# Kernel tuning notes

Measured on AMD Instinct MI355X. Metric: run time of the kernel, lower is better.

## Reference

```python
import jax, jax.numpy as jnp
import numpy as np

D_MODEL = 256
TOP_K = 32


def setup_inputs() -> dict:
    key = jax.random.key(0)
    k1, k2, k3 = jax.random.split(key, 3)
    query = jax.random.normal(k1, (4, 512, D_MODEL), dtype=jnp.float32)
    keys = jax.random.normal(k2, (65536, D_MODEL), dtype=jnp.float32)
    values = jax.random.normal(k3, (65536, D_MODEL), dtype=jnp.float32)
    return {"query": query, "keys": keys, "values": values}


def reference(query, keys, values):
    # query: [B, C, d], keys: [M, d], values: [M, d]
    reverse = False
    scale = D_MODEL ** (-0.5)
    scores = jnp.einsum("bcd,md->bcm", query, keys) * scale  # [B, C, M]
    if reverse:
        scores = -scores
    topk_scores, topk_indices = jax.lax.top_k(scores, TOP_K)  # [B, C, K]
    attn_weights = jax.nn.softmax(topk_scores, axis=-1)       # [B, C, K]
    retrieved = values[topk_indices]                           # [B, C, K, d]
    if reverse:
        retrieved = -retrieved
    aggregated = jnp.einsum("bckd,bck->bcd", retrieved, attn_weights)
    return aggregated
```

## Files before the change

### kernel.cpp

```cpp
#include <hip/hip_runtime.h>
#include <math.h>

#define D_MODEL 256
#define NQ 2048
#define M_KEYS 65536
#define CAP 512
#define RESCORE 64
#define TOPK 32
#define ZTHRESH 2.8f
#define QT 128
#define KPB 1024
#define KSTEP 32
#define NSTEP (KPB / KSTEP)
#define CAPQ 14

typedef _Float16 half8v __attribute__((ext_vector_type(8)));
typedef _Float16 half4v __attribute__((ext_vector_type(4)));
typedef float floatx4 __attribute__((ext_vector_type(4)));

__device__ __forceinline__ void async_load16(const _Float16* g, _Float16* l) {
  __builtin_amdgcn_global_load_lds(
      (const __attribute__((address_space(1))) void*)g,
      (__attribute__((address_space(3))) void*)l, 16, 0, 0);
}

__device__ __forceinline__ void issue_tile(const _Float16* __restrict__ kh, int row0,
                                           int sr0, int schunk, _Float16* dst, int tid) {
  const _Float16* src = kh + (size_t)(row0 + sr0) * D_MODEL + (schunk << 3);
  _Float16* d = dst + tid * 8;
#pragma unroll
  for (int jj = 0; jj < 4; ++jj)
    async_load16(src + (size_t)(jj * 8) * D_MODEL, d + jj * 2048);
}

__global__ __launch_bounds__(256) void cvt_f32_f16(const float* __restrict__ src,
                                                   _Float16* __restrict__ dst, int n4) {
  int i = blockIdx.x * 256 + threadIdx.x;
  if (i < n4) {
    const float4 v = ((const float4*)src)[i];
    half4v h = {(_Float16)v.x, (_Float16)v.y, (_Float16)v.z, (_Float16)v.w};
    ((half4v*)dst)[i] = h;
  }
}

__global__ __launch_bounds__(256) void qtau_kernel(const float* __restrict__ qf,
                                                   float* __restrict__ qtau) {
  const int lane = threadIdx.x & 63;
  const int q = blockIdx.x * 4 + (threadIdx.x >> 6);
  const float4 v = ((const float4*)(qf + (size_t)q * D_MODEL))[lane];
  float ss = v.x * v.x + v.y * v.y + v.z * v.z + v.w * v.w;
#pragma unroll
  for (int off = 32; off > 0; off >>= 1) ss += __shfl_down(ss, off);
  if (lane == 0) qtau[q] = ZTHRESH * sqrtf(ss);
}

__global__ __launch_bounds__(256, 2) void phase1_kernel(
    const _Float16* __restrict__ qh, const _Float16* __restrict__ kh,
    const float* __restrict__ qtau,
    float* __restrict__ cand_s, int* __restrict__ cand_i, int* __restrict__ cnt) {
  __shared__ __align__(16) char smem[65536];
  _Float16* qstage = (_Float16*)smem;
  _Float16* buf0 = (_Float16*)smem;
  _Float16* buf1 = (_Float16*)(smem + 16384);
  _Float16* buf2 = (_Float16*)(smem + 32768);
  float* qs = (float*)(smem + 49152);
  int* qi = (int*)(smem + 56320);
  int* qcnt = (int*)(smem + 63488);

  const int tid = threadIdx.x;
  const int lane = tid & 63;
  const int wave = tid >> 6;

  const int bid = blockIdx.x;
  const int xcd = bid & 7;
  const int j = bid >> 3;
  const int qbase = (j & 15) * QT;
  const int kstart0 = (xcd * 8 + (j >> 4)) * KPB;

  const int sr0 = tid >> 5;
  const int schunk = (tid & 31) ^ sr0;

  {
    const _Float16* src = qh + (size_t)(qbase + sr0) * D_MODEL + (schunk << 3);
    _Float16* d = qstage + tid * 8;
#pragma unroll
    for (int jj = 0; jj < 16; ++jj)
      async_load16(src + (size_t)(jj * 8) * D_MODEL, d + jj * 2048);
  }
  __syncthreads();

  const int lrow = lane & 15;
  const int g4 = lane >> 4;
  const int wr = wave << 5;
  const int lx = lrow & 7;

  half8v a[2][8];
#pragma unroll
  for (int mi = 0; mi < 2; ++mi) {
    const int row = wr + mi * 16 + lrow;
#pragma unroll
    for (int kk = 0; kk < 8; ++kk) {
      const int sw = ((kk << 2) + g4) ^ lx;
      a[mi][kk] = *(const half8v*)&qstage[row * D_MODEL + (sw << 3)];
    }
  }

  const int qrow0 = qbase + wr + (g4 << 2);
  float tq[8];
#pragma unroll
  for (int mi = 0; mi < 2; ++mi)
#pragma unroll
    for (int r = 0; r < 4; ++r)
      tq[mi * 4 + r] = qtau[qrow0 + mi * 16 + r];

  __syncthreads();

  if (tid < QT) qcnt[tid] = 0;

  issue_tile(kh, kstart0, sr0, schunk, buf0, tid);
  issue_tile(kh, kstart0 + KSTEP, sr0, schunk, buf1, tid);

  _Float16 *rdb = buf0, *nxb = buf1, *pfb = buf2;

#pragma unroll 1
  for (int s = 0; s < NSTEP; ++s) {
    if (s + 1 < NSTEP) {
      asm volatile("s_waitcnt vmcnt(4)" ::: "memory");
    } else {
      asm volatile("s_waitcnt vmcnt(0)" ::: "memory");
    }
    __builtin_amdgcn_s_barrier();
    __builtin_amdgcn_sched_barrier(0);

    if (s + 2 < NSTEP)
      issue_tile(kh, kstart0 + (s + 2) * KSTEP, sr0, schunk, pfb, tid);

    floatx4 acc[2][2] = {};
    __builtin_amdgcn_s_setprio(1);
#pragma unroll
    for (int kk = 0; kk < 8; ++kk) {
      const int sw = ((kk << 2) + g4) ^ lx;
      const half8v b0 = *(const half8v*)&rdb[lrow * D_MODEL + (sw << 3)];
      const half8v b1 = *(const half8v*)&rdb[(16 + lrow) * D_MODEL + (sw << 3)];
      acc[0][0] = __builtin_amdgcn_mfma_f32_16x16x32_f16(a[0][kk], b0, acc[0][0], 0, 0, 0);
      acc[0][1] = __builtin_amdgcn_mfma_f32_16x16x32_f16(a[0][kk], b1, acc[0][1], 0, 0, 0);
      acc[1][0] = __builtin_amdgcn_mfma_f32_16x16x32_f16(a[1][kk], b0, acc[1][0], 0, 0, 0);
      acc[1][1] = __builtin_amdgcn_mfma_f32_16x16x32_f16(a[1][kk], b1, acc[1][1], 0, 0, 0);
    }
    __builtin_amdgcn_s_setprio(0);

    const int kglob0 = kstart0 + s * KSTEP;
    const int qloc0 = wr + (g4 << 2);
#pragma unroll
    for (int mi = 0; mi < 2; ++mi) {
#pragma unroll
      for (int ni = 0; ni < 2; ++ni) {
#pragma unroll
        for (int r = 0; r < 4; ++r) {
          const float dot = acc[mi][ni][r];
          if (dot > tq[mi * 4 + r]) {
            const int ql = qloc0 + mi * 16 + r;
            const int kidx = kglob0 + ni * 16 + lrow;
            int p = atomicAdd(&qcnt[ql], 1);
            if (p < CAPQ) {
              qs[ql * CAPQ + p] = dot * 0.0625f;
              qi[ql * CAPQ + p] = kidx;
            } else {
              int pos = atomicAdd(&cnt[qbase + ql], 1);
              if (pos < CAP) {
                cand_s[(size_t)(qbase + ql) * CAP + pos] = dot * 0.0625f;
                cand_i[(size_t)(qbase + ql) * CAP + pos] = kidx;
              }
            }
          }
        }
      }
    }

    _Float16* t = rdb; rdb = nxb; nxb = pfb; pfb = t;
  }

  __syncthreads();
  if (tid < QT) {
    int n = qcnt[tid];
    if (n > CAPQ) n = CAPQ;
    if (n > 0) {
      const int q = qbase + tid;
      int base = atomicAdd(&cnt[q], n);
#pragma unroll 2
      for (int jj = 0; jj < n; ++jj) {
        int p = base + jj;
        if (p < CAP) {
          cand_s[(size_t)q * CAP + p] = qs[tid * CAPQ + jj];
          cand_i[(size_t)q * CAP + p] = qi[tid * CAPQ + jj];
        }
      }
    }
  }
}

__global__ __launch_bounds__(256) void phase2_kernel(
    const float* __restrict__ qf, const float* __restrict__ keys,
    const float* __restrict__ vals, const float* __restrict__ cand_s,
    const int* __restrict__ cand_i, const int* __restrict__ cnt,
    float* __restrict__ out) {
  __shared__ float sc[CAP];
  __shared__ int si[CAP];
  __shared__ float xs[RESCORE];
  __shared__ int xi[RESCORE];
  __shared__ float ew[TOPK];
  __shared__ float invsum;

  const int qid = blockIdx.x;
  const int tid = threadIdx.x;
  int c = cnt[qid];
  if (c > CAP) c = CAP;
  const int n = (c <= 256) ? 256 : CAP;

  for (int i = tid; i < n; i += 256) {
    bool valid = (i < c);
    sc[i] = valid ? cand_s[(size_t)qid * CAP + i] : -1e30f;
    si[i] = valid ? cand_i[(size_t)qid * CAP + i] : -1;
  }

  for (int k = 2; k <= n; k <<= 1) {
    for (int j = k >> 1; j > 0; j >>= 1) {
      __syncthreads();
      for (int t = tid; t < n; t += 256) {
        int p = t ^ j;
        if (p > t) {
          float a = sc[t], b = sc[p];
          bool desc = ((t & k) == 0);
          if (desc ? (a < b) : (a > b)) {
            sc[t] = b; sc[p] = a;
            int tmp = si[t]; si[t] = si[p]; si[p] = tmp;
          }
        }
      }
    }
  }
  __syncthreads();

  const int lane = tid & 63, wv = tid >> 6;
  const float4 qv = ((const float4*)(qf + (size_t)qid * D_MODEL))[lane];
#pragma unroll 4
  for (int cand = wv; cand < RESCORE; cand += 4) {
    int kidx = si[cand];
    float sres = -1e30f;
    if (kidx >= 0) {
      const float4 kv = ((const float4*)(keys + (size_t)kidx * D_MODEL))[lane];
      double p = (double)qv.x * kv.x + (double)qv.y * kv.y +
                 (double)qv.z * kv.z + (double)qv.w * kv.w;
#pragma unroll
      for (int off = 32; off > 0; off >>= 1) p += __shfl_down(p, off);
      sres = (float)(p * 0.0625);
    }
    if (lane == 0) { xs[cand] = sres; xi[cand] = kidx; }
  }
  __syncthreads();

  for (int k = 2; k <= RESCORE; k <<= 1) {
    for (int j = k >> 1; j > 0; j >>= 1) {
      __syncthreads();
      if (tid < RESCORE) {
        int t = tid, p = t ^ j;
        if (p > t) {
          float a = xs[t], b = xs[p];
          bool desc = ((t & k) == 0);
          if (desc ? (a < b) : (a > b)) {
            xs[t] = b; xs[p] = a;
            int tmp = xi[t]; xi[t] = xi[p]; xi[p] = tmp;
          }
        }
      }
    }
  }
  __syncthreads();

  if (tid < TOPK) ew[tid] = expf(xs[tid] - xs[0]);
  __syncthreads();
  if (tid == 0) {
    float s = 0.f;
    for (int i = 0; i < TOPK; ++i) s += ew[i];
    invsum = 1.0f / s;
  }
  __syncthreads();

  float acc = 0.f;
#pragma unroll
  for (int i = 0; i < TOPK; ++i)
    acc += (ew[i] * invsum) * vals[(size_t)xi[i] * D_MODEL + tid];
  out[(size_t)qid * D_MODEL + tid] = acc;
}

extern "C" void kernel_launch(void* const* d_in, const int* in_sizes, int n_in,
                              void* d_out, int out_size, void* d_ws, size_t ws_size,
                              hipStream_t stream) {
  const float* q = (const float*)d_in[0];
  const float* k = (const float*)d_in[1];
  const float* v = (const float*)d_in[2];
  float* out = (float*)d_out;

  char* ws = (char*)d_ws;
  _Float16* kh = (_Float16*)ws;
  _Float16* qh = (_Float16*)(ws + 33554432);
  float* cand_s = (float*)(ws + 34603008);
  int* cand_i = (int*)(ws + 38797312);
  int* cnt = (int*)(ws + 42991616);
  float* qtau = (float*)(ws + 42999808);

  hipMemsetAsync(cnt, 0, NQ * sizeof(int), stream);
  cvt_f32_f16<<<(M_KEYS * D_MODEL / 4 + 255) / 256, 256, 0, stream>>>(k, kh, M_KEYS * D_MODEL / 4);
  cvt_f32_f16<<<(NQ * D_MODEL / 4 + 255) / 256, 256, 0, stream>>>(q, qh, NQ * D_MODEL / 4);
  qtau_kernel<<<NQ / 4, 256, 0, stream>>>(q, qtau);

  phase1_kernel<<<(NQ / QT) * (M_KEYS / KPB), 256, 0, stream>>>(qh, kh, qtau, cand_s, cand_i, cnt);
  phase2_kernel<<<NQ, 256, 0, stream>>>(q, k, v, cand_s, cand_i, cnt, out);
}
```

Measured before the change: 285.6 us.

## Restructure phase1 into per-wave independent key streams with packed hit pool

Phase1 now has each wave stream its own 1024-key range through a private triple buffer of half-width tiles, which removes block-wide barriers from the main loop. Each block now covers 64 queries rather than 128, so every wave computes against all 64 queries. Hits are packed into 32-bit words (fp16 score plus a 16-bit key index), and the per-query shared pool grows to 32 entries to cut spills to global atomics. In exchange, the smaller query tile means keys are reread from L2 twice as often, and the candidate scores lose precision through fp16.

New measurement: 277.9 us. 2.7% less time.

```diff
diff --git a/kernel.cpp b/kernel.cpp
--- a/kernel.cpp
+++ b/kernel.cpp
@@ -8,11 +8,10 @@
 #define RESCORE 64
 #define TOPK 32
 #define ZTHRESH 2.8f
-#define QT 128
-#define KPB 1024
-#define KSTEP 32
-#define NSTEP (KPB / KSTEP)
-#define CAPQ 14
+#define QT 64
+#define KPW 1024
+#define NSUB 256
+#define CAPQ 32
 
 typedef _Float16 half8v __attribute__((ext_vector_type(8)));
 typedef _Float16 half4v __attribute__((ext_vector_type(4)));
@@ -24,13 +23,24 @@
       (__attribute__((address_space(3))) void*)l, 16, 0, 0);
 }
 
-__device__ __forceinline__ void issue_tile(const _Float16* __restrict__ kh, int row0,
-                                           int sr0, int schunk, _Float16* dst, int tid) {
-  const _Float16* src = kh + (size_t)(row0 + sr0) * D_MODEL + (schunk << 3);
-  _Float16* d = dst + tid * 8;
-#pragma unroll
-  for (int jj = 0; jj < 4; ++jj)
-    async_load16(src + (size_t)(jj * 8) * D_MODEL, d + jj * 2048);
+__device__ __forceinline__ unsigned pack_hit(float score, int kidx) {
+  _Float16 h = (_Float16)score;
+  unsigned short us;
+  __builtin_memcpy(&us, &h, 2);
+  return ((unsigned)us << 16) | (unsigned)(kidx & 0xFFFF);
+}
+
+__device__ __forceinline__ void issue_half(const _Float16* __restrict__ kh, int key0,
+                                           int hcol, _Float16* dst, int lane) {
+  const int l4 = lane >> 4;
+  const int lc = lane & 15;
+#pragma unroll
+  for (int j = 0; j < 4; ++j) {
+    const int row = 4 * j + l4;
+    const int sc = lc ^ (row & 7);
+    async_load16(kh + (size_t)(key0 + row) * D_MODEL + (hcol << 7) + (sc << 3),
+                 dst + lane * 8 + j * 512);
+  }
 }
 
 __global__ __launch_bounds__(256) void cvt_f32_f16(const float* __restrict__ src,
@@ -58,14 +68,10 @@
     const _Float16* __restrict__ qh, const _Float16* __restrict__ kh,
     const float* __restrict__ qtau,
     float* __restrict__ cand_s, int* __restrict__ cand_i, int* __restrict__ cnt) {
-  __shared__ __align__(16) char smem[65536];
+  __shared__ __align__(16) char smem[49152 + QT * CAPQ * 4 + QT * 4];
   _Float16* qstage = (_Float16*)smem;
-  _Float16* buf0 = (_Float16*)smem;
-  _Float16* buf1 = (_Float16*)(smem + 16384);
-  _Float16* buf2 = (_Float16*)(smem + 32768);
-  float* qs = (float*)(smem + 49152);
-  int* qi = (int*)(smem + 56320);
-  int* qcnt = (int*)(smem + 63488);
+  unsigned* qpool = (unsigned*)(smem + 49152);
+  int* qcnt = (int*)(smem + 49152 + QT * CAPQ * 4);
 
   const int tid = threadIdx.x;
   const int lane = tid & 63;
@@ -73,31 +79,31 @@
 
   const int bid = blockIdx.x;
   const int xcd = bid & 7;
-  const int j = bid >> 3;
-  const int qbase = (j & 15) * QT;
-  const int kstart0 = (xcd * 8 + (j >> 4)) * KPB;
-
-  const int sr0 = tid >> 5;
-  const int schunk = (tid & 31) ^ sr0;
+  const int loc = bid >> 3;
+  const int chunk = xcd * 2 + (loc & 1);
+  const int qbase = (loc >> 1) * QT;
+  const int kw0 = chunk * 4096 + wave * KPW;
 
   {
-    const _Float16* src = qh + (size_t)(qbase + sr0) * D_MODEL + (schunk << 3);
+    const int sr0 = tid >> 5;
+    const int sch = (tid & 31) ^ sr0;
+    const _Float16* src = qh + (size_t)(qbase + sr0) * D_MODEL + (sch << 3);
     _Float16* d = qstage + tid * 8;
 #pragma unroll
-    for (int jj = 0; jj < 16; ++jj)
-      async_load16(src + (size_t)(jj * 8) * D_MODEL, d + jj * 2048);
-  }
+    for (int j = 0; j < 8; ++j)
+      async_load16(src + (size_t)(j * 8) * D_MODEL, d + j * 2048);
+  }
+  if (tid < QT) qcnt[tid] = 0;
   __syncthreads();
 
   const int lrow = lane & 15;
   const int g4 = lane >> 4;
-  const int wr = wave << 5;
   const int lx = lrow & 7;
 
-  half8v a[2][8];
-#pragma unroll
-  for (int mi = 0; mi < 2; ++mi) {
-    const int row = wr + mi * 16 + lrow;
+  half8v a[4][8];
+#pragma unroll
+  for (int mi = 0; mi < 4; ++mi) {
+    const int row = mi * 16 + lrow;
 #pragma unroll
     for (int kk = 0; kk < 8; ++kk) {
       const int sw = ((kk << 2) + g4) ^ lx;
@@ -105,66 +111,61 @@
     }
   }
 
-  const int qrow0 = qbase + wr + (g4 << 2);
-  float tq[8];
-#pragma unroll
-  for (int mi = 0; mi < 2; ++mi)
-#pragma unroll
-    for (int r = 0; r < 4; ++r)
-      tq[mi * 4 + r] = qtau[qrow0 + mi * 16 + r];
-
-  __syncthreads();
-
-  if (tid < QT) qcnt[tid] = 0;
-
-  issue_tile(kh, kstart0, sr0, schunk, buf0, tid);
-  issue_tile(kh, kstart0 + KSTEP, sr0, schunk, buf1, tid);
-
-  _Float16 *rdb = buf0, *nxb = buf1, *pfb = buf2;
-
-#pragma unroll 1
-  for (int s = 0; s < NSTEP; ++s) {
-    if (s + 1 < NSTEP) {
-      asm volatile("s_waitcnt vmcnt(4)" ::: "memory");
-    } else {
-      asm volatile("s_waitcnt vmcnt(0)" ::: "memory");
-    }
-    __builtin_amdgcn_s_barrier();
+  float tq[16];
+#pragma unroll
+  for (int i = 0; i < 16; ++i)
+    tq[i] = qtau[qbase + ((i >> 2) << 4) + (g4 << 2) + (i & 3)];
+
+  __syncthreads();
+
+  _Float16* pA = (_Float16*)(smem + wave * 12288);
+  _Float16* pB = pA + 2048;
+  _Float16* pC = pB + 2048;
+
+  issue_half(kh, kw0, 0, pA, lane);
+  issue_half(kh, kw0, 1, pB, lane);
+  issue_half(kh, kw0 + 16, 0, pC, lane);
+
+  int roff[4];
+#pragma unroll
+  for (int c = 0; c < 4; ++c)
+    roff[c] = (lrow << 7) + (((((c << 2) + g4)) ^ lx) << 3);
+
+  floatx4 acc[4] = {};
+  const int nsub = (KPW / 16) * 2;
+
+#pragma unroll 2
+  for (int i = 0; i < nsub; ++i) {
+    if (i < nsub - 2)       asm volatile("s_waitcnt vmcnt(8)" ::: "memory");
+    else if (i == nsub - 2) asm volatile("s_waitcnt vmcnt(4)" ::: "memory");
+    else                    asm volatile("s_waitcnt vmcnt(0)" ::: "memory");
     __builtin_amdgcn_sched_barrier(0);
 
-    if (s + 2 < NSTEP)
-      issue_tile(kh, kstart0 + (s + 2) * KSTEP, sr0, schunk, pfb, tid);
-
-    floatx4 acc[2][2] = {};
+    const int kk0 = (i & 1) << 2;
     __builtin_amdgcn_s_setprio(1);
 #pragma unroll
-    for (int kk = 0; kk < 8; ++kk) {
-      const int sw = ((kk << 2) + g4) ^ lx;
-      const half8v b0 = *(const half8v*)&rdb[lrow * D_MODEL + (sw << 3)];
-      const half8v b1 = *(const half8v*)&rdb[(16 + lrow) * D_MODEL + (sw << 3)];
-      acc[0][0] = __builtin_amdgcn_mfma_f32_16x16x32_f16(a[0][kk], b0, acc[0][0], 0, 0, 0);
-      acc[0][1] = __builtin_amdgcn_mfma_f32_16x16x32_f16(a[0][kk], b1, acc[0][1], 0, 0, 0);
-      acc[1][0] = __builtin_amdgcn_mfma_f32_16x16x32_f16(a[1][kk], b0, acc[1][0], 0, 0, 0);
-      acc[1][1] = __builtin_amdgcn_mfma_f32_16x16x32_f16(a[1][kk], b1, acc[1][1], 0, 0, 0);
+    for (int c = 0; c < 4; ++c) {
+      const half8v b = *(const half8v*)&pA[roff[c]];
+      acc[0] = __builtin_amdgcn_mfma_f32_16x16x32_f16(a[0][kk0 + c], b, acc[0], 0, 0, 0);
+      acc[1] = __builtin_amdgcn_mfma_f32_16x16x32_f16(a[1][kk0 + c], b, acc[1], 0, 0, 0);
+      acc[2] = __builtin_amdgcn_mfma_f32_16x16x32_f16(a[2][kk0 + c], b, acc[2], 0, 0, 0);
+      acc[3] = __builtin_amdgcn_mfma_f32_16x16x32_f16(a[3][kk0 + c], b, acc[3], 0, 0, 0);
     }
     __builtin_amdgcn_s_setprio(0);
 
-    const int kglob0 = kstart0 + s * KSTEP;
-    const int qloc0 = wr + (g4 << 2);
-#pragma unroll
-    for (int mi = 0; mi < 2; ++mi) {
-#pragma unroll
-      for (int ni = 0; ni < 2; ++ni) {
+    if (i & 1) {
+      const int key0 = kw0 + (i >> 1) * 16;
+#pragma unroll
+      for (int mi = 0; mi < 4; ++mi) {
 #pragma unroll
         for (int r = 0; r < 4; ++r) {
-          const float dot = acc[mi][ni][r];
+          const float dot = acc[mi][r];
           if (dot > tq[mi * 4 + r]) {
-            const int ql = qloc0 + mi * 16 + r;
-            const int kidx = kglob0 + ni * 16 + lrow;
+            const int ql = mi * 16 + (g4 << 2) + r;
+            const int kidx = key0 + lrow;
             int p = atomicAdd(&qcnt[ql], 1);
             if (p < CAPQ) {
-              qs[ql * CAPQ + p] = dot * 0.0625f;
-              qi[ql * CAPQ + p] = kidx;
+              qpool[ql * CAPQ + p] = pack_hit(dot * 0.0625f, kidx);
             } else {
               int pos = atomicAdd(&cnt[qbase + ql], 1);
               if (pos < CAP) {
@@ -175,9 +176,16 @@
           }
         }
       }
-    }
-
-    _Float16* t = rdb; rdb = nxb; nxb = pfb; pfb = t;
+#pragma unroll
+      for (int mi = 0; mi < 4; ++mi) acc[mi] = (floatx4){0.f, 0.f, 0.f, 0.f};
+    }
+
+    if (i < nsub - 3) {
+      const int ni = i + 3;
+      __builtin_amdgcn_sched_barrier(0);
+      issue_half(kh, kw0 + (ni >> 1) * 16, ni & 1, pA, lane);
+    }
+    _Float16* t = pA; pA = pB; pB = pC; pC = t;
   }
 
   __syncthreads();
@@ -187,12 +195,15 @@
     if (n > 0) {
       const int q = qbase + tid;
       int base = atomicAdd(&cnt[q], n);
-#pragma unroll 2
-      for (int jj = 0; jj < n; ++jj) {
-        int p = base + jj;
-        if (p < CAP) {
-          cand_s[(size_t)q * CAP + p] = qs[tid * CAPQ + jj];
-          cand_i[(size_t)q * CAP + p] = qi[tid * CAPQ + jj];
+      for (int j = 0; j < n; ++j) {
+        int pos = base + j;
+        if (pos < CAP) {
+          unsigned pk = qpool[tid * CAPQ + j];
+          unsigned short us = (unsigned short)(pk >> 16);
+          _Float16 hs;
+          __builtin_memcpy(&hs, &us, 2);
+          cand_s[(size_t)q * CAP + pos] = (float)hs;
+          cand_i[(size_t)q * CAP + pos] = (int)(pk & 0xFFFFu);
         }
       }
     }
@@ -314,6 +325,6 @@
   cvt_f32_f16<<<(NQ * D_MODEL / 4 + 255) / 256, 256, 0, stream>>>(q, qh, NQ * D_MODEL / 4);
   qtau_kernel<<<NQ / 4, 256, 0, stream>>>(q, qtau);
 
-  phase1_kernel<<<(NQ / QT) * (M_KEYS / KPB), 256, 0, stream>>>(qh, kh, qtau, cand_s, cand_i, cnt);
+  phase1_kernel<<<(NQ / QT) * (M_KEYS / 4096), 256, 0, stream>>>(qh, kh, qtau, cand_s, cand_i, cnt);
   phase2_kernel<<<NQ, 256, 0, stream>>>(q, k, v, cand_s, cand_i, cnt, out);
 }
```
